# Kernel tuning notes

Measured on AMD Instinct MI355X. Metric: run time of the kernel, lower is better.

## Reference

```python
import jax, jax.numpy as jnp
import numpy as np


def setup_inputs() -> dict:
    key = jax.random.key(0)
    x = jax.random.normal(key, (2, 2048, 512), dtype=jnp.float32)
    return {"x": x, "num_heads": 8, "kernel_size": 63}


def reference(x, num_heads, kernel_size):
    # NATTEN na1d with dilation=1: each query attends to a kernel_size window
    # centered at its position; near the sequence edges the window is shifted
    # (clamped) to stay fully inside [0, L), so every query sees exactly K keys.
    B, L, D = x.shape
    H = num_heads
    hd = D // H
    K = kernel_size
    scale = float(hd) ** -0.5

    qkv = x.reshape(B, L, H, hd)  # q == k == v == reshaped x

    # window start per query position, clamped so the window fits in bounds
    start = jnp.clip(jnp.arange(L) - K // 2, 0, L - K)          # (L,)
    idx = start[:, None] + jnp.arange(K)                         # (L, K)

    kv = qkv[:, idx]                                             # (B, L, K, H, hd)
    scores = jnp.einsum("blhd,blkhd->bhlk", qkv, kv) * scale     # (B, H, L, K)
    attn = jax.nn.softmax(scores, axis=-1)
    out = jnp.einsum("bhlk,blkhd->blhd", attn, kv)               # (B, L, H, hd)
    return out.reshape(B, L, D)
```

## Files before the change

kernel.cpp:

```cpp
#include <hip/hip_runtime.h>

#define B_ 2
#define L_ 2048
#define H_ 8
#define HD 64
#define K_ 63
#define TQ 64
#define NT (L_ / TQ)
#define ROWS 128
#define EXPC 0.1803368801111204f

typedef __attribute__((ext_vector_type(8))) short bf16x8;
typedef __attribute__((ext_vector_type(4))) float f32x4;
typedef __attribute__((ext_vector_type(4))) unsigned short u16x4;

__device__ inline unsigned short f2bf(float f) {
    unsigned u = __float_as_uint(f);
    unsigned r = ((u >> 16) & 1u) + 0x7FFFu;
    return (unsigned short)((u + r) >> 16);
}

__global__ __launch_bounds__(256) void natten1d_mfma(
    const float* __restrict__ x, float* __restrict__ out)
{
    __shared__ unsigned short kv_sh [ROWS * 64];
    __shared__ unsigned short kvT_sh[64 * ROWS];
    __shared__ unsigned short pt_sh [4 * 16 * ROWS];

    const int bid = blockIdx.x;
    const int wid = (bid & 7) * (B_ * H_ * NT / 8) + (bid >> 3);
    const int bh  = wid / NT;
    const int t   = wid % NT;
    const int b   = bh / H_;
    const int h   = bh % H_;
    const int l0  = t * TQ;
    const int key_base = min(max(l0 - K_ / 2, 0), L_ - K_);
    const int qoff     = l0 - key_base;

    const int tid = threadIdx.x;

    const float4* xb = (const float4*)x + (size_t)b * (L_ * H_ * HD / 4) + h * (HD / 4);
    #pragma unroll
    for (int it = 0; it < 2; ++it) {
        const int mt = tid + it * 256;
        const int rg = mt >> 4;
        const int d4 = mt & 15;
        const int r0 = rg * 4;
        unsigned short bf[4][4];
        #pragma unroll
        for (int rr = 0; rr < 4; ++rr) {
            const int g = key_base + r0 + rr;
            float4 v = make_float4(0.f, 0.f, 0.f, 0.f);
            if (g < L_) v = xb[(size_t)g * (H_ * HD / 4) + d4];
            bf[rr][0] = f2bf(v.x); bf[rr][1] = f2bf(v.y);
            bf[rr][2] = f2bf(v.z); bf[rr][3] = f2bf(v.w);
            const int r = r0 + rr;
            *(u16x4*)&kv_sh[r * 64 + (((d4 >> 1) ^ (r & 7)) << 3) + (d4 & 1) * 4] =
                (u16x4){bf[rr][0], bf[rr][1], bf[rr][2], bf[rr][3]};
        }
        #pragma unroll
        for (int e = 0; e < 4; ++e) {
            const int d = d4 * 4 + e;
            *(u16x4*)&kvT_sh[d * 128 + (((rg >> 1) ^ (d & 15)) << 3) + ((rg & 1) << 2)] =
                (u16x4){bf[0][e], bf[1][e], bf[2][e], bf[3][e]};
        }
    }
    __syncthreads();

    const int wave = tid >> 6;
    const int lane = tid & 63;
    const int lq = lane & 15;
    const int lg = lane >> 4;

    bf16x8 aq[2];
    {
        const int qrow = qoff + wave * 16 + lq;
        aq[0] = *(const bf16x8*)&kv_sh[qrow * 64 + ((lg ^ (qrow & 7)) << 3)];
        aq[1] = *(const bf16x8*)&kv_sh[qrow * 64 + (((4 + lg) ^ (qrow & 7)) << 3)];
    }
    f32x4 acc[8];
    #pragma unroll
    for (int nb = 0; nb < 8; ++nb) acc[nb] = (f32x4){0.f, 0.f, 0.f, 0.f};
    #pragma unroll
    for (int nb = 0; nb < 8; ++nb) {
        const int krow = nb * 16 + lq;
        const bf16x8 b0 = *(const bf16x8*)&kv_sh[krow * 64 + ((lg ^ (krow & 7)) << 3)];
        const bf16x8 b1 = *(const bf16x8*)&kv_sh[krow * 64 + (((4 + lg) ^ (krow & 7)) << 3)];
        acc[nb] = __builtin_amdgcn_mfma_f32_16x16x32_bf16(aq[0], b0, acc[nb], 0, 0, 0);
        acc[nb] = __builtin_amdgcn_mfma_f32_16x16x32_bf16(aq[1], b1, acc[nb], 0, 0, 0);
    }

    float rz[4];
    #pragma unroll
    for (int r = 0; r < 4; ++r) {
        const int q    = wave * 16 + lg * 4 + r;
        const int soff = min(max(l0 + q - K_ / 2, 0), L_ - K_) - key_base;
        float mrow = -1e30f;
        #pragma unroll
        for (int nb = 0; nb < 8; ++nb) {
            const int col = nb * 16 + lq;
            float s = acc[nb][r];
            s = ((unsigned)(col - soff) <= (unsigned)(K_ - 1)) ? s : -1e30f;
            acc[nb][r] = s;
            mrow = fmaxf(mrow, s);
        }
        #pragma unroll
        for (int o = 1; o <= 8; o <<= 1) mrow = fmaxf(mrow, __shfl_xor(mrow, o));
        float z = 0.f;
        #pragma unroll
        for (int nb = 0; nb < 8; ++nb) {
            const float e = exp2f((acc[nb][r] - mrow) * EXPC);
            acc[nb][r] = e;
            z += e;
        }
        #pragma unroll
        for (int o = 1; o <= 8; o <<= 1) z += __shfl_xor(z, o);
        rz[r] = 1.0f / z;
    }

    unsigned short* ptw = &pt_sh[wave * 16 * 128];
    #pragma unroll
    for (int nb = 0; nb < 8; ++nb) {
        #pragma unroll
        for (int r = 0; r < 4; ++r) {
            const int q = lg * 4 + r;
            ptw[q * 128 + ((((nb * 2) + (lq >> 3)) ^ (q & 15)) << 3) + (lq & 7)]
                = f2bf(acc[nb][r]);
        }
    }

    bf16x8 ap[4];
    #pragma unroll
    for (int kc = 0; kc < 4; ++kc)
        ap[kc] = *(const bf16x8*)&ptw[lq * 128 + (((kc * 4 + lg) ^ (lq & 15)) << 3)];
    f32x4 o4[4];
    #pragma unroll
    for (int nb = 0; nb < 4; ++nb) o4[nb] = (f32x4){0.f, 0.f, 0.f, 0.f};
    #pragma unroll
    for (int nb = 0; nb < 4; ++nb) {
        const int d = nb * 16 + lq;
        #pragma unroll
        for (int kc = 0; kc < 4; ++kc) {
            const bf16x8 bv = *(const bf16x8*)&kvT_sh[d * 128 + (((kc * 4 + lg) ^ (d & 15)) << 3)];
            o4[nb] = __builtin_amdgcn_mfma_f32_16x16x32_bf16(ap[kc], bv, o4[nb], 0, 0, 0);
        }
    }

    #pragma unroll
    for (int nb = 0; nb < 4; ++nb) {
        const int d = nb * 16 + lq;
        #pragma unroll
        for (int r = 0; r < 4; ++r) {
            const int q = wave * 16 + lg * 4 + r;
            out[((size_t)(b * L_ + l0 + q) * H_ + h) * HD + d] = o4[nb][r] * rz[r];
        }
    }
}

extern "C" void kernel_launch(void* const* d_in, const int* in_sizes, int n_in,
                              void* d_out, int out_size, void* d_ws, size_t ws_size,
                              hipStream_t stream)
{
    const float* x = (const float*)d_in[0];
    float* out = (float*)d_out;
    natten1d_mfma<<<dim3(B_ * H_ * NT), dim3(256), 0, stream>>>(x, out);
}
```

Baseline: 13.14 us.

## Restrict per-wave key window to 96 rows and transpose QK^T for row-local softmax

Each wave now computes scores only over a 96-key band aligned to its query block instead of all 128 staged keys, cutting QK^T MFMAs from 16 to 12 and PV MFMAs from 16 to 12 per wave. The score MFMA operands are swapped so each lane owns one query's scores, which lets the softmax reduce mostly in registers with two cross-lane shuffles instead of four per row. Normalization is folded into the probabilities before the bf16 pack. The fp32 to bf16 conversion uses the packed v_cvt_pk_bf16_f32 instruction, global loads are batched ahead of the LDS stores, and launch bounds now request 2 blocks per SM. The window-offset logic is more intricate, so edge positions risk masking mistakes.

```diff
diff --git a/kernel.cpp b/kernel.cpp
--- a/kernel.cpp
+++ b/kernel.cpp
@@ -12,20 +12,19 @@
 
 typedef __attribute__((ext_vector_type(8))) short bf16x8;
 typedef __attribute__((ext_vector_type(4))) float f32x4;
-typedef __attribute__((ext_vector_type(4))) unsigned short u16x4;
 
-__device__ inline unsigned short f2bf(float f) {
-    unsigned u = __float_as_uint(f);
-    unsigned r = ((u >> 16) & 1u) + 0x7FFFu;
-    return (unsigned short)((u + r) >> 16);
+__device__ inline unsigned cvt_pk_bf16(float lo, float hi) {
+    unsigned r;
+    asm("v_cvt_pk_bf16_f32 %0, %1, %2" : "=v"(r) : "v"(lo), "v"(hi));
+    return r;
 }
 
-__global__ __launch_bounds__(256) void natten1d_mfma(
+__global__ __launch_bounds__(256, 2) void natten1d_mfma(
     const float* __restrict__ x, float* __restrict__ out)
 {
     __shared__ unsigned short kv_sh [ROWS * 64];
     __shared__ unsigned short kvT_sh[64 * ROWS];
-    __shared__ unsigned short pt_sh [4 * 16 * ROWS];
+    __shared__ unsigned short pt_sh [4 * 16 * 128];
 
     const int bid = blockIdx.x;
     const int wid = (bid & 7) * (B_ * H_ * NT / 8) + (bid >> 3);
@@ -38,31 +37,44 @@
     const int qoff     = l0 - key_base;
 
     const int tid = threadIdx.x;
+    const int d4  = tid & 15;
+    const int rg0 = tid >> 4;
 
     const float4* xb = (const float4*)x + (size_t)b * (L_ * H_ * HD / 4) + h * (HD / 4);
+    float4 ld[8];
     #pragma unroll
-    for (int it = 0; it < 2; ++it) {
-        const int mt = tid + it * 256;
-        const int rg = mt >> 4;
-        const int d4 = mt & 15;
-        const int r0 = rg * 4;
-        unsigned short bf[4][4];
+    for (int m = 0; m < 2; ++m) {
+        const int rg = rg0 + m * 16;
         #pragma unroll
         for (int rr = 0; rr < 4; ++rr) {
-            const int g = key_base + r0 + rr;
-            float4 v = make_float4(0.f, 0.f, 0.f, 0.f);
-            if (g < L_) v = xb[(size_t)g * (H_ * HD / 4) + d4];
-            bf[rr][0] = f2bf(v.x); bf[rr][1] = f2bf(v.y);
-            bf[rr][2] = f2bf(v.z); bf[rr][3] = f2bf(v.w);
-            const int r = r0 + rr;
-            *(u16x4*)&kv_sh[r * 64 + (((d4 >> 1) ^ (r & 7)) << 3) + (d4 & 1) * 4] =
-                (u16x4){bf[rr][0], bf[rr][1], bf[rr][2], bf[rr][3]};
+            const int g = key_base + rg * 4 + rr;
+            ld[m * 4 + rr] = (g < L_) ? xb[(size_t)g * (H_ * HD / 4) + d4]
+                                      : make_float4(0.f, 0.f, 0.f, 0.f);
+        }
+    }
+    #pragma unroll
+    for (int m = 0; m < 2; ++m) {
+        const int rg = rg0 + m * 16;
+        #pragma unroll
+        for (int rr = 0; rr < 4; ++rr) {
+            const int r = rg * 4 + rr;
+            const float4 v = ld[m * 4 + rr];
+            uint2 w;
+            w.x = cvt_pk_bf16(v.x, v.y);
+            w.y = cvt_pk_bf16(v.z, v.w);
+            *(uint2*)&kv_sh[r * 64 + (((d4 >> 1) ^ (r & 7)) << 3) + (d4 & 1) * 4] = w;
         }
         #pragma unroll
         for (int e = 0; e < 4; ++e) {
             const int d = d4 * 4 + e;
-            *(u16x4*)&kvT_sh[d * 128 + (((rg >> 1) ^ (d & 15)) << 3) + ((rg & 1) << 2)] =
-                (u16x4){bf[0][e], bf[1][e], bf[2][e], bf[3][e]};
+            const float* f0 = (const float*)&ld[m * 4 + 0];
+            const float* f1 = (const float*)&ld[m * 4 + 1];
+            const float* f2 = (const float*)&ld[m * 4 + 2];
+            const float* f3 = (const float*)&ld[m * 4 + 3];
+            uint2 w;
+            w.x = cvt_pk_bf16(f0[e], f1[e]);
+            w.y = cvt_pk_bf16(f2[e], f3[e]);
+            *(uint2*)&kvT_sh[d * 128 + (((rg >> 1) ^ (d & 15)) << 3) + ((rg & 1) << 2)] = w;
         }
     }
     __syncthreads();
@@ -72,76 +84,81 @@
     const int lq = lane & 15;
     const int lg = lane >> 4;
 
-    bf16x8 aq[2];
-    {
-        const int qrow = qoff + wave * 16 + lq;
-        aq[0] = *(const bf16x8*)&kv_sh[qrow * 64 + ((lg ^ (qrow & 7)) << 3)];
-        aq[1] = *(const bf16x8*)&kv_sh[qrow * 64 + (((4 + lg) ^ (qrow & 7)) << 3)];
-    }
-    f32x4 acc[8];
+    const int q0    = wave * 16;
+    const int soff0 = min(max(l0 + q0 - K_ / 2, 0), L_ - K_) - key_base;
+    const int wb    = min(soff0 & ~15, ROWS - 96);
+    const int qrow  = qoff + q0 + lq;
+    const int soffq = min(max(l0 + q0 + lq - K_ / 2, 0), L_ - K_) - key_base;
+    const int cbase = wb + lg * 4 - soffq;
+
+    bf16x8 bq[2];
+    bq[0] = *(const bf16x8*)&kv_sh[qrow * 64 + ((lg ^ (qrow & 7)) << 3)];
+    bq[1] = *(const bf16x8*)&kv_sh[qrow * 64 + (((4 + lg) ^ (qrow & 7)) << 3)];
+
+    f32x4 acc[6];
     #pragma unroll
-    for (int nb = 0; nb < 8; ++nb) acc[nb] = (f32x4){0.f, 0.f, 0.f, 0.f};
+    for (int nb = 0; nb < 6; ++nb) acc[nb] = (f32x4){0.f, 0.f, 0.f, 0.f};
     #pragma unroll
-    for (int nb = 0; nb < 8; ++nb) {
-        const int krow = nb * 16 + lq;
-        const bf16x8 b0 = *(const bf16x8*)&kv_sh[krow * 64 + ((lg ^ (krow & 7)) << 3)];
-        const bf16x8 b1 = *(const bf16x8*)&kv_sh[krow * 64 + (((4 + lg) ^ (krow & 7)) << 3)];
-        acc[nb] = __builtin_amdgcn_mfma_f32_16x16x32_bf16(aq[0], b0, acc[nb], 0, 0, 0);
-        acc[nb] = __builtin_amdgcn_mfma_f32_16x16x32_bf16(aq[1], b1, acc[nb], 0, 0, 0);
+    for (int nb = 0; nb < 6; ++nb) {
+        const int krow = wb + nb * 16 + lq;
+        const bf16x8 a0 = *(const bf16x8*)&kv_sh[krow * 64 + ((lg ^ (krow & 7)) << 3)];
+        const bf16x8 a1 = *(const bf16x8*)&kv_sh[krow * 64 + (((4 + lg) ^ (krow & 7)) << 3)];
+        acc[nb] = __builtin_amdgcn_mfma_f32_16x16x32_bf16(a0, bq[0], acc[nb], 0, 0, 0);
+        acc[nb] = __builtin_amdgcn_mfma_f32_16x16x32_bf16(a1, bq[1], acc[nb], 0, 0, 0);
     }
 
-    float rz[4];
+    float mx = -1e30f;
     #pragma unroll
-    for (int r = 0; r < 4; ++r) {
-        const int q    = wave * 16 + lg * 4 + r;
-        const int soff = min(max(l0 + q - K_ / 2, 0), L_ - K_) - key_base;
-        float mrow = -1e30f;
+    for (int nb = 0; nb < 6; ++nb) {
         #pragma unroll
-        for (int nb = 0; nb < 8; ++nb) {
-            const int col = nb * 16 + lq;
-            float s = acc[nb][r];
-            s = ((unsigned)(col - soff) <= (unsigned)(K_ - 1)) ? s : -1e30f;
+        for (int r = 0; r < 4; ++r) {
+            const bool valid = (unsigned)(cbase + nb * 16 + r) < (unsigned)K_;
+            const float s = valid ? acc[nb][r] : -1e30f;
             acc[nb][r] = s;
-            mrow = fmaxf(mrow, s);
+            mx = fmaxf(mx, s);
         }
+    }
+    mx = fmaxf(mx, __shfl_xor(mx, 16));
+    mx = fmaxf(mx, __shfl_xor(mx, 32));
+    float z = 0.f;
+    #pragma unroll
+    for (int nb = 0; nb < 6; ++nb) {
         #pragma unroll
-        for (int o = 1; o <= 8; o <<= 1) mrow = fmaxf(mrow, __shfl_xor(mrow, o));
-        float z = 0.f;
-        #pragma unroll
-        for (int nb = 0; nb < 8; ++nb) {
-            const float e = exp2f((acc[nb][r] - mrow) * EXPC);
+        for (int r = 0; r < 4; ++r) {
+            const float e = exp2f((acc[nb][r] - mx) * EXPC);
             acc[nb][r] = e;
             z += e;
         }
-        #pragma unroll
-        for (int o = 1; o <= 8; o <<= 1) z += __shfl_xor(z, o);
-        rz[r] = 1.0f / z;
     }
+    z += __shfl_xor(z, 16);
+    z += __shfl_xor(z, 32);
+    const float rz = 1.0f / z;
 
     unsigned short* ptw = &pt_sh[wave * 16 * 128];
     #pragma unroll
-    for (int nb = 0; nb < 8; ++nb) {
-        #pragma unroll
-        for (int r = 0; r < 4; ++r) {
-            const int q = lg * 4 + r;
-            ptw[q * 128 + ((((nb * 2) + (lq >> 3)) ^ (q & 15)) << 3) + (lq & 7)]
-                = f2bf(acc[nb][r]);
-        }
+    for (int nb = 0; nb < 6; ++nb) {
+        uint2 w;
+        w.x = cvt_pk_bf16(acc[nb][0] * rz, acc[nb][1] * rz);
+        w.y = cvt_pk_bf16(acc[nb][2] * rz, acc[nb][3] * rz);
+        const int g = nb * 2 + (lg >> 1);
+        *(uint2*)&ptw[lq * 128 + ((g ^ lq) << 3) + ((lg & 1) << 2)] = w;
     }
 
-    bf16x8 ap[4];
+    bf16x8 ap[3];
     #pragma unroll
-    for (int kc = 0; kc < 4; ++kc)
-        ap[kc] = *(const bf16x8*)&ptw[lq * 128 + (((kc * 4 + lg) ^ (lq & 15)) << 3)];
+    for (int kc = 0; kc < 3; ++kc)
+        ap[kc] = *(const bf16x8*)&ptw[lq * 128 + (((kc * 4 + lg) ^ lq) << 3)];
     f32x4 o4[4];
     #pragma unroll
     for (int nb = 0; nb < 4; ++nb) o4[nb] = (f32x4){0.f, 0.f, 0.f, 0.f};
+    const int kg0 = wb >> 3;
     #pragma unroll
     for (int nb = 0; nb < 4; ++nb) {
         const int d = nb * 16 + lq;
         #pragma unroll
-        for (int kc = 0; kc < 4; ++kc) {
-            const bf16x8 bv = *(const bf16x8*)&kvT_sh[d * 128 + (((kc * 4 + lg) ^ (d & 15)) << 3)];
+        for (int kc = 0; kc < 3; ++kc) {
+            const bf16x8 bv =
+                *(const bf16x8*)&kvT_sh[d * 128 + (((kg0 + kc * 4 + lg) ^ (d & 15)) << 3)];
             o4[nb] = __builtin_amdgcn_mfma_f32_16x16x32_bf16(ap[kc], bv, o4[nb], 0, 0, 0);
         }
     }
@@ -151,8 +168,8 @@
         const int d = nb * 16 + lq;
         #pragma unroll
         for (int r = 0; r < 4; ++r) {
-            const int q = wave * 16 + lg * 4 + r;
-            out[((size_t)(b * L_ + l0 + q) * H_ + h) * HD + d] = o4[nb][r] * rz[r];
+            const int q = q0 + lg * 4 + r;
+            out[((size_t)(b * L_ + l0 + q) * H_ + h) * HD + d] = o4[nb][r];
         }
     }
 }
```

After: 11.15 us. -15.1%, faster.
